# Kernel tuning notes

Measured on AMD Instinct MI355X. Metric: run time of the kernel, lower is better.

The kernel has to match this reference:

```python
import jax, jax.numpy as jnp
import numpy as np
from functools import partial

N = 8192          # nodes
E = 131072        # directed edges (avg degree 16)
INPUT_DIM = 256
INTERM = 32
LATENT = 64       # m
MAX_ITERS = 32    # fixed unroll of the rejection-sampling while-loop


def setup_inputs() -> dict:
    key = jax.random.key(0)
    ks = jax.random.split(key, 8)
    X = jax.random.normal(ks[0], (N, INPUT_DIM), dtype=jnp.float32)
    edge_index = jax.random.randint(ks[1], (2, E), 0, N, dtype=jnp.int64)
    W1 = jax.random.normal(ks[2], (INPUT_DIM, INTERM), dtype=jnp.float32) / np.sqrt(INPUT_DIM)
    b1 = jnp.zeros((INTERM,), jnp.float32)
    W_mu = jax.random.normal(ks[3], (INTERM, LATENT), dtype=jnp.float32) / np.sqrt(INTERM)
    b_mu = jnp.zeros((LATENT,), jnp.float32)
    W_k = jax.random.normal(ks[4], (INTERM, 1), dtype=jnp.float32) / np.sqrt(INTERM)
    b_k = jnp.zeros((1,), jnp.float32)
    return {"X": X, "edge_index": edge_index, "W1": W1, "b1": b1,
            "W_mu": W_mu, "b_mu": b_mu, "W_k": W_k, "b_k": b_k}


def _gcn(H, src, dst, norm, W, b):
    # GCNConv: out = D^-1/2 (A+I) D^-1/2 (H W) + b, edge-list form
    HW = H @ W
    msg = HW[src] * norm[:, None]
    return jax.ops.segment_sum(msg, dst, num_segments=N) + b


def _sample_w(kappas, key):
    # Wood's rejection sampling for the vMF mixing scalar w (fixed-iteration scan)
    m = LATENT
    s = jnp.sqrt(4.0 * kappas ** 2 + (m - 1) ** 2)
    b = (-2.0 * kappas + s) / (m - 1)
    a = (m - 1 + 2.0 * kappas + s) / 4.0
    d = 4.0 * a * b / (1.0 + b) - (m - 1) * np.log(m - 1)

    def step(carry, k):
        w, sampled = carry
        kb, ku = jax.random.split(k)
        eps = jax.random.beta(kb, (m - 1) / 2.0, (m - 1) / 2.0, (kappas.shape[0],))
        denom = 1.0 - (1.0 - b) * eps
        w_prop = (1.0 - (1.0 + b) * eps) / denom
        t = 2.0 * a * b / denom
        u = jax.random.uniform(ku, (kappas.shape[0],))
        acc = (m - 1) * jnp.log(t) - t + d >= jnp.log(u)
        w = jnp.where(sampled, w, w_prop)   # keep first accepted proposal
        sampled = sampled | acc
        return (w, sampled), None

    init = (jnp.zeros_like(kappas), jnp.zeros(kappas.shape, dtype=bool))
    (w, _), _ = jax.lax.scan(step, init, jax.random.split(key, MAX_ITERS))
    return w


def _sample_vMF(mus, kappas, key):
    m = LATENT
    kw, kv = jax.random.split(key)
    w = _sample_w(kappas, kw)[:, None]                     # [N,1]
    v = jax.random.normal(kv, (mus.shape[0], m - 1), dtype=mus.dtype)
    v = v / jnp.linalg.norm(v, axis=1, keepdims=True)
    z = jnp.concatenate([w, jnp.sqrt(jnp.clip(1.0 - w ** 2, 0.0)) * v], axis=-1)
    # householder reflection mapping e1 -> mu
    e = jnp.zeros((1, m), dtype=mus.dtype).at[0, 0].set(1.0)
    u = e - mus
    u = u / (jnp.linalg.norm(u, axis=-1, keepdims=True) + 1e-8)
    return z - 2.0 * jnp.sum(z * u, axis=-1, keepdims=True) * u


def reference(X, edge_index, W1, b1, W_mu, b_mu, W_k, b_k):
    src0, dst0 = edge_index[0], edge_index[1]
    loops = jnp.arange(N, dtype=src0.dtype)
    src = jnp.concatenate([src0, loops])
    dst = jnp.concatenate([dst0, loops])
    deg = jax.ops.segment_sum(jnp.ones(src.shape[0], X.dtype), dst, num_segments=N)
    dinv = jnp.where(deg > 0, jax.lax.rsqrt(deg), 0.0)
    norm = dinv[src] * dinv[dst]

    H = jax.nn.relu(_gcn(X, src, dst, norm, W1, b1))       # dropout in eval mode
    mus = _gcn(H, src, dst, norm, W_mu, b_mu)
    kap = jax.nn.softplus(jnp.squeeze(_gcn(H, src, dst, norm, W_k, b_k), -1))
    mus = mus / (jnp.linalg.norm(mus, axis=-1, keepdims=True) + 1e-12)

    Z = _sample_vMF(mus, kap, jax.random.key(42))
    ZZt = Z @ Z.T                                           # [N,N]
    return ZZt, mus, kap
```

## Files before the change

### kernel.cpp

```cpp
#include <hip/hip_runtime.h>
#include <hip/hip_bf16.h>

#pragma clang fp contract(off)

#define NN 8192
#define NE 131072
#define DIN 256
#define DH 32
#define DL 64

typedef unsigned int u32;
typedef __bf16 bf16x8 __attribute__((ext_vector_type(8)));
typedef float f32x4 __attribute__((ext_vector_type(4)));

struct Key { u32 a, b; };

__device__ __forceinline__ u32 rotl32(u32 x, int d) { return (x << d) | (x >> (32 - d)); }

__device__ __forceinline__ void tf2x32(u32 k0, u32 k1, u32& x0, u32& x1) {
  u32 k2 = k0 ^ k1 ^ 0x1BD11BDAu;
  x0 += k0; x1 += k1;
  x0 += x1; x1 = rotl32(x1, 13); x1 ^= x0;
  x0 += x1; x1 = rotl32(x1, 15); x1 ^= x0;
  x0 += x1; x1 = rotl32(x1, 26); x1 ^= x0;
  x0 += x1; x1 = rotl32(x1, 6);  x1 ^= x0;
  x0 += k1; x1 += k2 + 1u;
  x0 += x1; x1 = rotl32(x1, 17); x1 ^= x0;
  x0 += x1; x1 = rotl32(x1, 29); x1 ^= x0;
  x0 += x1; x1 = rotl32(x1, 16); x1 ^= x0;
  x0 += x1; x1 = rotl32(x1, 24); x1 ^= x0;
  x0 += k2; x1 += k0 + 2u;
  x0 += x1; x1 = rotl32(x1, 13); x1 ^= x0;
  x0 += x1; x1 = rotl32(x1, 15); x1 ^= x0;
  x0 += x1; x1 = rotl32(x1, 26); x1 ^= x0;
  x0 += x1; x1 = rotl32(x1, 6);  x1 ^= x0;
  x0 += k0; x1 += k1 + 3u;
  x0 += x1; x1 = rotl32(x1, 17); x1 ^= x0;
  x0 += x1; x1 = rotl32(x1, 29); x1 ^= x0;
  x0 += x1; x1 = rotl32(x1, 16); x1 ^= x0;
  x0 += x1; x1 = rotl32(x1, 24); x1 ^= x0;
  x0 += k1; x1 += k2 + 4u;
  x0 += x1; x1 = rotl32(x1, 13); x1 ^= x0;
  x0 += x1; x1 = rotl32(x1, 15); x1 ^= x0;
  x0 += x1; x1 = rotl32(x1, 26); x1 ^= x0;
  x0 += x1; x1 = rotl32(x1, 6);  x1 ^= x0;
  x0 += k2; x1 += k0 + 5u;
}

__device__ __forceinline__ Key fold(Key k, u32 i) {
  u32 x0 = 0u, x1 = i; tf2x32(k.a, k.b, x0, x1);
  Key r; r.a = x0; r.b = x1; return r;
}
__device__ __forceinline__ u32 pbits(Key k, u32 i) {
  u32 x0 = 0u, x1 = i; tf2x32(k.a, k.b, x0, x1);
  return x0 ^ x1;
}


__device__ __forceinline__ float xla_logf(float x) {
  if (x == 0.0f) return -__builtin_huge_valf();
  u32 bits = __float_as_uint(x);
  float ef = (float)((int)(bits >> 23) - 126);
  float m = __uint_as_float((bits & 0x007fffffu) | 0x3f000000u);
  if (m < 0.707106781186547524f) { ef = ef - 1.0f; m = m + m; }
  m = m - 1.0f;
  float z = m * m;
  float y = 7.0376836292e-2f;
  y = fmaf(y, m, -1.1514610310e-1f);
  y = fmaf(y, m, 1.1676998740e-1f);
  y = fmaf(y, m, -1.2420140846e-1f);
  y = fmaf(y, m, 1.4249322787e-1f);
  y = fmaf(y, m, -1.6668057665e-1f);
  y = fmaf(y, m, 2.0000714765e-1f);
  y = fmaf(y, m, -2.4999993993e-1f);
  y = fmaf(y, m, 3.3333331174e-1f);
  y = y * m;
  y = y * z;
  y = fmaf(ef, -2.12194440e-4f, y);
  y = fmaf(-0.5f, z, y);
  float r = m + y;
  r = fmaf(ef, 0.693359375f, r);
  return r;
}

__device__ __forceinline__ float xla_expf(float x) {
  x = fminf(x, 88.3762626647950f);
  x = fmaxf(x, -88.3762626647949f);
  float fx = fmaf(x, 1.44269504088896341f, 0.5f);
  fx = floorf(fx);
  x = fmaf(-fx, 0.693359375f, x);
  x = fmaf(fx, 2.12194440e-4f, x);
  float z = x * x;
  float y = 1.9875691500e-4f;
  y = fmaf(y, x, 1.3981999507e-3f);
  y = fmaf(y, x, 8.3334519073e-3f);
  y = fmaf(y, x, 4.1665795894e-2f);
  y = fmaf(y, x, 1.6666665459e-1f);
  y = fmaf(y, x, 5.0000001201e-1f);
  y = fmaf(y, z, x);
  y = y + 1.0f;
  int n = (int)fx;
  float p2n = __uint_as_float((u32)(n + 127) << 23);
  return y * p2n;
}

__device__ __forceinline__ float xla_log1pf(float x) {
  float u = x + 1.0f;
  if (u == 1.0f) return x;
  return xla_logf(u) * (x / (u - 1.0f));
}

__device__ __forceinline__ float u01_from_bits(u32 b) {
  return __uint_as_float((b >> 9) | 0x3f800000u) - 1.0f;
}
__device__ __forceinline__ float jax_uniform_scalar(Key k) {
  float f = u01_from_bits(pbits(k, 0u));
  return fmaxf(0.0f, f);
}

__device__ __forceinline__ float erfinv_f32(float x) {
  float w = -xla_log1pf(-(x * x));
  float p;
  if (w < 5.0f) {
    w = w - 2.5f;
    p = 2.81022636e-08f;
    p = fmaf(p, w, 3.43273939e-07f);
    p = fmaf(p, w, -3.5233877e-06f);
    p = fmaf(p, w, -4.39150654e-06f);
    p = fmaf(p, w, 0.00021858087f);
    p = fmaf(p, w, -0.00125372503f);
    p = fmaf(p, w, -0.00417768164f);
    p = fmaf(p, w, 0.246640727f);
    p = fmaf(p, w, 1.50140941f);
  } else {
    w = sqrtf(w) - 3.0f;
    p = -0.000200214257f;
    p = fmaf(p, w, 0.000100950558f);
    p = fmaf(p, w, 0.00134934322f);
    p = fmaf(p, w, -0.00367342844f);
    p = fmaf(p, w, 0.00573950773f);
    p = fmaf(p, w, -0.0076224613f);
    p = fmaf(p, w, 0.00943887047f);
    p = fmaf(p, w, 1.00167406f);
    p = fmaf(p, w, 2.83297682f);
  }
  return p * x;
}

__device__ __forceinline__ float normal_from_bits(u32 b) {
  float f = u01_from_bits(b);
  const float lo = -0.99999994f;
  float u = fmaxf(lo, fmaf(f, 2.0f, lo));
  return 1.4142135623730951f * erfinv_f32(u);
}

__device__ float loggamma31_5(Key k) {
  const float dd = 31.5f - (1.0f / 3.0f);
  const float cc = 1.0f / sqrtf(9.0f * dd);
  Key key = fold(k, 0u);
  float X = 0.0f, V = 1.0f, U = 2.0f;
  for (int it = 0; it < 64; ++it) {
    bool c1 = U >= fmaf(-0.0331f, X * X, 1.0f);
    bool c2 = xla_logf(U) >= fmaf(dd, (1.0f - V) + xla_logf(V), X * 0.5f);
    if (!(c1 && c2)) break;
    Key xk = fold(key, 1u);
    Key Uk = fold(key, 2u);
    key = fold(key, 0u);
    float x = 0.0f, v = -1.0f;
    for (int j = 0; j < 32 && v <= 0.0f; ++j) {
      Key sk = fold(xk, 1u);
      xk = fold(xk, 0u);
      x = normal_from_bits(pbits(sk, 0u));
      v = fmaf(x, cc, 1.0f);
    }
    X = x * x; V = (v * v) * v;
    U = jax_uniform_scalar(Uk);
  }
  return xla_logf(V) + xla_logf(dd);
}

__device__ __forceinline__ float wave_sum(float v) {
  for (int d = 1; d < 64; d <<= 1) v += __shfl_xor(v, d, 64);
  return v;
}


__global__ void count_k(const int* __restrict__ ei, u32* __restrict__ cnt) {
  int e = blockIdx.x * blockDim.x + threadIdx.x;
  if (e < NE) atomicAdd(&cnt[ei[NE + e]], 1u);
}

__global__ void scan_k(const u32* __restrict__ cnt, u32* __restrict__ off, float* __restrict__ dinv) {
  __shared__ u32 part[256];
  int t = threadIdx.x;
  int base = t * 32;
  u32 s = 0;
  for (int i = 0; i < 32; ++i) s += cnt[base + i];
  part[t] = s;
  __syncthreads();
  if (t == 0) {
    u32 acc = 0;
    for (int i = 0; i < 256; ++i) { u32 v = part[i]; part[i] = acc; acc += v; }
  }
  __syncthreads();
  u32 acc = part[t];
  for (int i = 0; i < 32; ++i) {
    off[base + i] = acc;
    u32 c = cnt[base + i];
    acc += c;
    dinv[base + i] = 1.0f / sqrtf((float)(c + 1u));
  }
  if (t == 255) off[NN] = acc;
}

__global__ void fill_k(const int* __restrict__ ei, const u32* __restrict__ off,
                       u32* __restrict__ fl, u32* __restrict__ csr) {
  int e = blockIdx.x * blockDim.x + threadIdx.x;
  if (e < NE) {
    int d = ei[NE + e];
    u32 p = off[d] + atomicAdd(&fl[d], 1u);
    csr[p] = (u32)e;
  }
}

__global__ void sort_k(const u32* __restrict__ off, u32* __restrict__ csr) {
  int n = blockIdx.x * blockDim.x + threadIdx.x;
  if (n >= NN) return;
  u32 s = off[n], e2 = off[n + 1];
  for (u32 i = s + 1; i < e2; ++i) {
    u32 v = csr[i]; u32 j = i;
    while (j > s && csr[j - 1] > v) { csr[j] = csr[j - 1]; --j; }
    csr[j] = v;
  }
}

__global__ __launch_bounds__(256) void mm_xw1_k(const float* __restrict__ X,
                                                const float* __restrict__ W1,
                                                float* __restrict__ XW) {
  __shared__ float w[DIN * DH];
  for (int i = threadIdx.x; i < DIN * DH; i += 256) w[i] = W1[i];
  __syncthreads();
  int f = threadIdx.x & 31, r0 = threadIdx.x >> 5;
  int base = blockIdx.x * 32;
  for (int pass = 0; pass < 4; ++pass) {
    int r = base + r0 + pass * 8;
    const float4* xr = reinterpret_cast<const float4*>(X + (size_t)r * DIN);
    float acc = 0.0f;
    for (int k4 = 0; k4 < DIN / 4; ++k4) {
      float4 xv = xr[k4];
      int k = k4 * 4;
      acc = fmaf(xv.x, w[(k + 0) * DH + f], acc);
      acc = fmaf(xv.y, w[(k + 1) * DH + f], acc);
      acc = fmaf(xv.z, w[(k + 2) * DH + f], acc);
      acc = fmaf(xv.w, w[(k + 3) * DH + f], acc);
    }
    XW[(size_t)r * DH + f] = acc;
  }
}

__global__ void agg_h_k(const float* __restrict__ XW, const u32* __restrict__ off,
                        const u32* __restrict__ csr, const int* __restrict__ ei,
                        const float* __restrict__ dinv, const float* __restrict__ b1,
                        float* __restrict__ H) {
  int idx = blockIdx.x * blockDim.x + threadIdx.x;
  int n = idx >> 5, f = idx & 31;
  if (n >= NN) return;
  float dn = dinv[n];
  float acc = 0.0f;
  u32 s0 = off[n], s1 = off[n + 1];
  for (u32 p = s0; p < s1; ++p) {
    int e = (int)csr[p];
    int s = ei[e];
    acc += XW[s * DH + f] * (dinv[s] * dn);
  }
  acc += XW[n * DH + f] * (dn * dn);
  acc += b1[f];
  H[n * DH + f] = fmaxf(acc, 0.0f);
}

__global__ void mm_h_k(const float* __restrict__ H, const float* __restrict__ Wmu,
                       const float* __restrict__ Wk, float* __restrict__ HWmu,
                       float* __restrict__ HWk) {
  __shared__ float wm[DH * DL];
  __shared__ float wk[DH];
  for (int i = threadIdx.x; i < DH * DL; i += 256) wm[i] = Wmu[i];
  if (threadIdx.x < DH) wk[threadIdx.x] = Wk[threadIdx.x];
  __syncthreads();
  int f = threadIdx.x & 63, l = threadIdx.x >> 6;
  int n = blockIdx.x * 4 + l;
  const float* h = H + n * DH;
  float acc = 0.0f;
  for (int k = 0; k < DH; ++k) acc = fmaf(h[k], wm[k * DL + f], acc);
  HWmu[(size_t)n * DL + f] = acc;
  if (f == 0) {
    float a2 = 0.0f;
    for (int k = 0; k < DH; ++k) a2 = fmaf(h[k], wk[k], a2);
    HWk[n] = a2;
  }
}

__global__ void agg_mu_k(const float* __restrict__ HW, const u32* __restrict__ off,
                         const u32* __restrict__ csr, const int* __restrict__ ei,
                         const float* __restrict__ dinv, const float* __restrict__ bmu,
                         float* __restrict__ out) {
  int idx = blockIdx.x * blockDim.x + threadIdx.x;
  int n = idx >> 6, f = idx & 63;
  if (n >= NN) return;
  float dn = dinv[n], acc = 0.0f;
  for (u32 p = off[n]; p < off[n + 1]; ++p) {
    int e = (int)csr[p]; int s = ei[e];
    acc += HW[(size_t)s * DL + f] * (dinv[s] * dn);
  }
  acc += HW[(size_t)n * DL + f] * (dn * dn);
  out[(size_t)n * DL + f] = acc + bmu[f];
}

__global__ void agg_kap_k(const float* __restrict__ HWk, const u32* __restrict__ off,
                          const u32* __restrict__ csr, const int* __restrict__ ei,
                          const float* __restrict__ dinv, const float* __restrict__ bk,
                          float* __restrict__ kap, float* __restrict__ outKA) {
  int n = blockIdx.x * blockDim.x + threadIdx.x;
  if (n >= NN) return;
  float dn = dinv[n], acc = 0.0f;
  for (u32 p = off[n]; p < off[n + 1]; ++p) {
    int e = (int)csr[p]; int s = ei[e];
    acc += HWk[s] * (dinv[s] * dn);
  }
  acc += HWk[n] * (dn * dn);
  acc += bk[0];
  float sp = fmaxf(acc, 0.0f) + xla_log1pf(xla_expf(-fabsf(acc)));
  kap[n] = sp; outKA[n] = sp;
}

__global__ void norm_mus_k(const float* __restrict__ musraw, float* __restrict__ mus,
                           float* __restrict__ outMU) {
  int gid = blockIdx.x * blockDim.x + threadIdx.x;
  int n = gid >> 6, lane = threadIdx.x & 63;
  if (n >= NN) return;
  float v = musraw[(size_t)n * DL + lane];
  float nm = sqrtf(wave_sum(v * v)) + 1e-12f;
  float r = v / nm;
  mus[(size_t)n * DL + lane] = r;
  outMU[(size_t)n * DL + lane] = r;
}


__global__ void build_keys_k(u32* __restrict__ ktab) {
  if (threadIdx.x != 0 || blockIdx.x != 0) return;
  Key root; root.a = 0u; root.b = 42u;
  Key kw = fold(root, 0u);
  Key kv = fold(root, 1u);
  ktab[192] = kv.a; ktab[193] = kv.b;
  for (int t = 0; t < 32; ++t) {
    Key kt = fold(kw, (u32)t);
    Key kb = fold(kt, 0u);
    Key ku = fold(kt, 1u);
    Key ka = fold(kb, 0u);
    Key kbb = fold(kb, 1u);
    ktab[6 * t + 0] = ka.a;  ktab[6 * t + 1] = ka.b;
    ktab[6 * t + 2] = kbb.a; ktab[6 * t + 3] = kbb.b;
    ktab[6 * t + 4] = ku.a;  ktab[6 * t + 5] = ku.b;
  }
}

__global__ void sample_w_k(const float* __restrict__ kap, const u32* __restrict__ ktab,
                           float* __restrict__ wv) {
  int n = blockIdx.x * blockDim.x + threadIdx.x;
  if (n >= NN) return;
  float kappa = kap[n];
  float kk = kappa * kappa;
  float s  = sqrtf(fmaf(4.0f, kk, 3969.0f));
  float bb = fmaf(-2.0f, kappa, s) / 63.0f;
  float aa = (fmaf(2.0f, kappa, 63.0f) + s) / 4.0f;
  float dd = (4.0f * aa) * bb / (1.0f + bb) - 261.01748776266657f;
  float w = 0.0f;
  for (int t = 0; t < 32; ++t) {
    const u32* kt = ktab + 6 * t;
    Key ka; ka.a = kt[0]; ka.b = kt[1];
    Key kb; kb.a = kt[2]; kb.b = kt[3];
    Key ku; ku.a = kt[4]; ku.b = kt[5];
    Key sa = fold(ka, (u32)n);
    Key sb = fold(kb, (u32)n);
    float lga = loggamma31_5(sa);
    float lgb = loggamma31_5(sb);
    float mx = fmaxf(lga, lgb);
    float ea = xla_expf(lga - mx), eb = xla_expf(lgb - mx);
    float eps = ea / (ea + eb);
    float u = fmaxf(0.0f, u01_from_bits(pbits(ku, (u32)n)));
    float denom = fmaf(-(1.0f - bb), eps, 1.0f);
    w = fmaf(-(1.0f + bb), eps, 1.0f) / denom;
    float tt = (2.0f * aa) * bb / denom;
    float lt = xla_logf(tt);
    float margin = fmaf(63.0f, lt, -tt) + dd;
    if (margin >= xla_logf(u)) break;
  }
  wv[n] = w;
}

__global__ void z_k(const float* __restrict__ mus, const float* __restrict__ wv,
                    const u32* __restrict__ ktab, __bf16* __restrict__ Zh) {
  int gid = blockIdx.x * blockDim.x + threadIdx.x;
  int n = gid >> 6, lane = threadIdx.x & 63;
  if (n >= NN) return;
  Key kv; kv.a = ktab[192]; kv.b = ktab[193];
  float vj = 0.0f;
  if (lane >= 1) {
    u32 idx = (u32)(n * 63 + (lane - 1));
    vj = normal_from_bits(pbits(kv, idx));
  }
  float vn = sqrtf(wave_sum(vj * vj));
  vj = vj / vn;
  float w = wv[n];
  float zj = (lane == 0) ? w : sqrtf(fmaxf(1.0f - w * w, 0.0f)) * vj;
  float mu = mus[(size_t)n * DL + lane];
  float uh = ((lane == 0) ? 1.0f : 0.0f) - mu;
  float un = sqrtf(wave_sum(uh * uh)) + 1e-8f;
  uh = uh / un;
  float dot = wave_sum(zj * uh);
  float zf = zj - 2.0f * dot * uh;
  Zh[(size_t)n * DL + lane] = (__bf16)zf;
}

__global__ __launch_bounds__(256) void zzt_k(const __bf16* __restrict__ Zh,
                                             float* __restrict__ out) {
  int wave = threadIdx.x >> 6;
  int lane = threadIdx.x & 63;
  int bi = blockIdx.y * 128 + (wave >> 1) * 64;
  int bj = blockIdx.x * 128 + (wave & 1) * 64;
  int r = lane & 15, kh = lane >> 4;
  bf16x8 afr[4][2], bfr[4][2];
#pragma unroll
  for (int ig = 0; ig < 4; ++ig)
#pragma unroll
    for (int kk = 0; kk < 2; ++kk) {
      afr[ig][kk] = *reinterpret_cast<const bf16x8*>(
          Zh + (size_t)(bi + ig * 16 + r) * DL + kk * 32 + kh * 8);
      bfr[ig][kk] = *reinterpret_cast<const bf16x8*>(
          Zh + (size_t)(bj + ig * 16 + r) * DL + kk * 32 + kh * 8);
    }
  f32x4 acc[4][4];
#pragma unroll
  for (int ig = 0; ig < 4; ++ig)
#pragma unroll
    for (int jg = 0; jg < 4; ++jg) {
      acc[ig][jg] = (f32x4){0.0f, 0.0f, 0.0f, 0.0f};
      acc[ig][jg] = __builtin_amdgcn_mfma_f32_16x16x32_bf16(
          afr[ig][0], bfr[jg][0], acc[ig][jg], 0, 0, 0);
      acc[ig][jg] = __builtin_amdgcn_mfma_f32_16x16x32_bf16(
          afr[ig][1], bfr[jg][1], acc[ig][jg], 0, 0, 0);
    }
#pragma unroll
  for (int ig = 0; ig < 4; ++ig)
#pragma unroll
    for (int jg = 0; jg < 4; ++jg) {
      size_t rowbase = (size_t)(bi + ig * 16 + kh * 4);
#pragma unroll
      for (int rr = 0; rr < 4; ++rr) {
        out[(rowbase + rr) * NN + (bj + jg * 16 + r)] = acc[ig][jg][rr];
      }
    }
}


extern "C" void kernel_launch(void* const* d_in, const int* in_sizes, int n_in,
                              void* d_out, int out_size, void* d_ws, size_t ws_size,
                              hipStream_t stream) {
  const float* X   = (const float*)d_in[0];
  const int*   ei  = (const int*)d_in[1];
  const float* W1  = (const float*)d_in[2];
  const float* b1  = (const float*)d_in[3];
  const float* Wmu = (const float*)d_in[4];
  const float* bmu = (const float*)d_in[5];
  const float* Wk  = (const float*)d_in[6];
  const float* bk  = (const float*)d_in[7];

  char* wp = (char*)d_ws;
  auto alloc = [&](size_t bytes) -> char* {
    char* p = wp; wp += (bytes + 255) & ~(size_t)255; return p;
  };
  u32* cnt    = (u32*)alloc((size_t)NN * 4);
  u32* fill   = (u32*)alloc((size_t)NN * 4);
  u32* off    = (u32*)alloc((size_t)(NN + 1) * 4);
  u32* csr    = (u32*)alloc((size_t)NE * 4);
  u32* ktab   = (u32*)alloc(256 * 4);
  float* dinv = (float*)alloc((size_t)NN * 4);
  float* XW1  = (float*)alloc((size_t)NN * DH * 4);
  float* H    = (float*)alloc((size_t)NN * DH * 4);
  float* HWmu = (float*)alloc((size_t)NN * DL * 4);
  float* HWk  = (float*)alloc((size_t)NN * 4);
  float* musr = (float*)alloc((size_t)NN * DL * 4);
  float* mus  = (float*)alloc((size_t)NN * DL * 4);
  float* kap  = (float*)alloc((size_t)NN * 4);
  float* wv   = (float*)alloc((size_t)NN * 4);
  __bf16* Zh  = (__bf16*)alloc((size_t)NN * DL * 2);

  float* outZZ = (float*)d_out;
  float* outMU = outZZ + (size_t)NN * NN;
  float* outKA = outMU + (size_t)NN * DL;

  hipMemsetAsync(cnt, 0, (size_t)NN * 4, stream);
  hipMemsetAsync(fill, 0, (size_t)NN * 4, stream);
  build_keys_k<<<1, 64, 0, stream>>>(ktab);
  count_k<<<NE / 256, 256, 0, stream>>>(ei, cnt);
  scan_k<<<1, 256, 0, stream>>>(cnt, off, dinv);
  fill_k<<<NE / 256, 256, 0, stream>>>(ei, off, fill, csr);
  sort_k<<<NN / 256, 256, 0, stream>>>(off, csr);
  mm_xw1_k<<<NN / 32, 256, 0, stream>>>(X, W1, XW1);
  agg_h_k<<<NN * DH / 256, 256, 0, stream>>>(XW1, off, csr, ei, dinv, b1, H);
  mm_h_k<<<NN / 4, 256, 0, stream>>>(H, Wmu, Wk, HWmu, HWk);
  agg_mu_k<<<NN * DL / 256, 256, 0, stream>>>(HWmu, off, csr, ei, dinv, bmu, musr);
  agg_kap_k<<<NN / 256, 256, 0, stream>>>(HWk, off, csr, ei, dinv, bk, kap, outKA);
  norm_mus_k<<<NN * DL / 256, 256, 0, stream>>>(musr, mus, outMU);
  sample_w_k<<<NN / 256, 256, 0, stream>>>(kap, ktab, wv);
  z_k<<<NN * DL / 256, 256, 0, stream>>>(mus, wv, ktab, Zh);
  dim3 g(64, 64);
  zzt_k<<<g, 256, 0, stream>>>(Zh, outZZ);
}
```

Before: 270.1 us.

## Fuse GCN aggregation stages, inline RNG keys, and vectorize ZZt stores

The first GCN aggregation is fused with the Wmu/Wk projection, so H lives in shared memory and never goes to global memory. The mu and kappa aggregations share one launch by splitting on block index, and so do the mu normalisation and the vMF w sampling. The key-table kernel is removed by deriving keys inline, and the two memsets are merged into one that relies on the adjacent cnt/fill allocations. The ZZt output now uses float4 stores with swapped row and column indexing, which is correct only because Z·Zᵀ is symmetric. This cuts launch count and intermediate traffic and the number of store instructions on the large output.

```diff
diff --git a/kernel.cpp b/kernel.cpp
--- a/kernel.cpp
+++ b/kernel.cpp
@@ -234,6 +234,7 @@
   }
 }
 
+
 __global__ __launch_bounds__(256) void mm_xw1_k(const float* __restrict__ X,
                                                 const float* __restrict__ W1,
                                                 float* __restrict__ XW) {
@@ -258,151 +259,142 @@
   }
 }
 
-__global__ void agg_h_k(const float* __restrict__ XW, const u32* __restrict__ off,
-                        const u32* __restrict__ csr, const int* __restrict__ ei,
-                        const float* __restrict__ dinv, const float* __restrict__ b1,
-                        float* __restrict__ H) {
-  int idx = blockIdx.x * blockDim.x + threadIdx.x;
-  int n = idx >> 5, f = idx & 31;
-  if (n >= NN) return;
-  float dn = dinv[n];
-  float acc = 0.0f;
-  u32 s0 = off[n], s1 = off[n + 1];
-  for (u32 p = s0; p < s1; ++p) {
-    int e = (int)csr[p];
-    int s = ei[e];
-    acc += XW[s * DH + f] * (dinv[s] * dn);
-  }
-  acc += XW[n * DH + f] * (dn * dn);
-  acc += b1[f];
-  H[n * DH + f] = fmaxf(acc, 0.0f);
-}
-
-__global__ void mm_h_k(const float* __restrict__ H, const float* __restrict__ Wmu,
-                       const float* __restrict__ Wk, float* __restrict__ HWmu,
-                       float* __restrict__ HWk) {
+__global__ __launch_bounds__(256) void agg_h_mm_k(const float* __restrict__ XW,
+                                                  const u32* __restrict__ off,
+                                                  const u32* __restrict__ csr,
+                                                  const int* __restrict__ ei,
+                                                  const float* __restrict__ dinv,
+                                                  const float* __restrict__ b1,
+                                                  const float* __restrict__ Wmu,
+                                                  const float* __restrict__ Wk,
+                                                  float* __restrict__ HWmu,
+                                                  float* __restrict__ HWk) {
+  __shared__ float Hs[8][DH];
   __shared__ float wm[DH * DL];
   __shared__ float wk[DH];
   for (int i = threadIdx.x; i < DH * DL; i += 256) wm[i] = Wmu[i];
   if (threadIdx.x < DH) wk[threadIdx.x] = Wk[threadIdx.x];
+  int nl = threadIdx.x >> 5, f = threadIdx.x & 31;
+  int n = blockIdx.x * 8 + nl;
+  {
+    float dn = dinv[n];
+    float acc = 0.0f;
+    u32 s0 = off[n], s1 = off[n + 1];
+    for (u32 p = s0; p < s1; ++p) {
+      int e = (int)csr[p];
+      int s = ei[e];
+      acc += XW[(size_t)s * DH + f] * (dinv[s] * dn);
+    }
+    acc += XW[(size_t)n * DH + f] * (dn * dn);
+    acc += b1[f];
+    Hs[nl][f] = fmaxf(acc, 0.0f);
+  }
   __syncthreads();
-  int f = threadIdx.x & 63, l = threadIdx.x >> 6;
-  int n = blockIdx.x * 4 + l;
-  const float* h = H + n * DH;
-  float acc = 0.0f;
-  for (int k = 0; k < DH; ++k) acc = fmaf(h[k], wm[k * DL + f], acc);
-  HWmu[(size_t)n * DL + f] = acc;
-  if (f == 0) {
-    float a2 = 0.0f;
-    for (int k = 0; k < DH; ++k) a2 = fmaf(h[k], wk[k], a2);
-    HWk[n] = a2;
-  }
-}
-
-__global__ void agg_mu_k(const float* __restrict__ HW, const u32* __restrict__ off,
-                         const u32* __restrict__ csr, const int* __restrict__ ei,
-                         const float* __restrict__ dinv, const float* __restrict__ bmu,
-                         float* __restrict__ out) {
-  int idx = blockIdx.x * blockDim.x + threadIdx.x;
-  int n = idx >> 6, f = idx & 63;
-  if (n >= NN) return;
-  float dn = dinv[n], acc = 0.0f;
-  for (u32 p = off[n]; p < off[n + 1]; ++p) {
-    int e = (int)csr[p]; int s = ei[e];
-    acc += HW[(size_t)s * DL + f] * (dinv[s] * dn);
-  }
-  acc += HW[(size_t)n * DL + f] * (dn * dn);
-  out[(size_t)n * DL + f] = acc + bmu[f];
-}
-
-__global__ void agg_kap_k(const float* __restrict__ HWk, const u32* __restrict__ off,
-                          const u32* __restrict__ csr, const int* __restrict__ ei,
-                          const float* __restrict__ dinv, const float* __restrict__ bk,
-                          float* __restrict__ kap, float* __restrict__ outKA) {
-  int n = blockIdx.x * blockDim.x + threadIdx.x;
-  if (n >= NN) return;
-  float dn = dinv[n], acc = 0.0f;
-  for (u32 p = off[n]; p < off[n + 1]; ++p) {
-    int e = (int)csr[p]; int s = ei[e];
-    acc += HWk[s] * (dinv[s] * dn);
-  }
-  acc += HWk[n] * (dn * dn);
-  acc += bk[0];
-  float sp = fmaxf(acc, 0.0f) + xla_log1pf(xla_expf(-fabsf(acc)));
-  kap[n] = sp; outKA[n] = sp;
-}
-
-__global__ void norm_mus_k(const float* __restrict__ musraw, float* __restrict__ mus,
-                           float* __restrict__ outMU) {
+  int f2 = threadIdx.x & 63, l = threadIdx.x >> 6;
+#pragma unroll
+  for (int rep = 0; rep < 2; ++rep) {
+    int nl2 = l + rep * 4;
+    int n2 = blockIdx.x * 8 + nl2;
+    const float* h = Hs[nl2];
+    float acc = 0.0f;
+    for (int k = 0; k < DH; ++k) acc = fmaf(h[k], wm[k * DL + f2], acc);
+    HWmu[(size_t)n2 * DL + f2] = acc;
+    if (f2 == 0) {
+      float a2 = 0.0f;
+      for (int k = 0; k < DH; ++k) a2 = fmaf(h[k], wk[k], a2);
+      HWk[n2] = a2;
+    }
+  }
+}
+
+__global__ void agg_mu_kap_k(const float* __restrict__ HW, const float* __restrict__ HWk,
+                             const u32* __restrict__ off, const u32* __restrict__ csr,
+                             const int* __restrict__ ei, const float* __restrict__ dinv,
+                             const float* __restrict__ bmu, const float* __restrict__ bk,
+                             float* __restrict__ musr, float* __restrict__ kap,
+                             float* __restrict__ outKA) {
+  int bid = blockIdx.x;
+  if (bid < 2048) {
+    int idx = bid * 256 + threadIdx.x;
+    int n = idx >> 6, f = idx & 63;
+    float dn = dinv[n], acc = 0.0f;
+    for (u32 p = off[n]; p < off[n + 1]; ++p) {
+      int e = (int)csr[p]; int s = ei[e];
+      acc += HW[(size_t)s * DL + f] * (dinv[s] * dn);
+    }
+    acc += HW[(size_t)n * DL + f] * (dn * dn);
+    musr[(size_t)n * DL + f] = acc + bmu[f];
+  } else {
+    int n = (bid - 2048) * 256 + threadIdx.x;
+    if (n >= NN) return;
+    float dn = dinv[n], acc = 0.0f;
+    for (u32 p = off[n]; p < off[n + 1]; ++p) {
+      int e = (int)csr[p]; int s = ei[e];
+      acc += HWk[s] * (dinv[s] * dn);
+    }
+    acc += HWk[n] * (dn * dn);
+    acc += bk[0];
+    float sp = fmaxf(acc, 0.0f) + xla_log1pf(xla_expf(-fabsf(acc)));
+    kap[n] = sp; outKA[n] = sp;
+  }
+}
+
+__global__ void norm_sample_k(const float* __restrict__ musraw, float* __restrict__ mus,
+                              float* __restrict__ outMU, const float* __restrict__ kap,
+                              float* __restrict__ wv) {
+  int bid = blockIdx.x;
+  if (bid < 2048) {
+    int gid = bid * 256 + threadIdx.x;
+    int n = gid >> 6, lane = threadIdx.x & 63;
+    float v = musraw[(size_t)n * DL + lane];
+    float nm = sqrtf(wave_sum(v * v)) + 1e-12f;
+    float r = v / nm;
+    mus[(size_t)n * DL + lane] = r;
+    outMU[(size_t)n * DL + lane] = r;
+  } else {
+    int n = (bid - 2048) * 256 + threadIdx.x;
+    if (n >= NN) return;
+    Key root; root.a = 0u; root.b = 42u;
+    Key kw = fold(root, 0u);
+    float kappa = kap[n];
+    float kk = kappa * kappa;
+    float s  = sqrtf(fmaf(4.0f, kk, 3969.0f));
+    float bb = fmaf(-2.0f, kappa, s) / 63.0f;
+    float aa = (fmaf(2.0f, kappa, 63.0f) + s) / 4.0f;
+    float dd = (4.0f * aa) * bb / (1.0f + bb) - 261.01748776266657f;
+    float w = 0.0f;
+    for (int t = 0; t < 32; ++t) {
+      Key kt = fold(kw, (u32)t);
+      Key kb = fold(kt, 0u);
+      Key ku = fold(kt, 1u);
+      Key ka = fold(kb, 0u);
+      Key kbb = fold(kb, 1u);
+      Key sa = fold(ka, (u32)n);
+      Key sb = fold(kbb, (u32)n);
+      float lga = loggamma31_5(sa);
+      float lgb = loggamma31_5(sb);
+      float mx = fmaxf(lga, lgb);
+      float ea = xla_expf(lga - mx), eb = xla_expf(lgb - mx);
+      float eps = ea / (ea + eb);
+      float u = fmaxf(0.0f, u01_from_bits(pbits(ku, (u32)n)));
+      float denom = fmaf(-(1.0f - bb), eps, 1.0f);
+      w = fmaf(-(1.0f + bb), eps, 1.0f) / denom;
+      float tt = (2.0f * aa) * bb / denom;
+      float lt = xla_logf(tt);
+      float margin = fmaf(63.0f, lt, -tt) + dd;
+      if (margin >= xla_logf(u)) break;
+    }
+    wv[n] = w;
+  }
+}
+
+__global__ void z_k(const float* __restrict__ mus, const float* __restrict__ wv,
+                    __bf16* __restrict__ Zh) {
   int gid = blockIdx.x * blockDim.x + threadIdx.x;
   int n = gid >> 6, lane = threadIdx.x & 63;
   if (n >= NN) return;
-  float v = musraw[(size_t)n * DL + lane];
-  float nm = sqrtf(wave_sum(v * v)) + 1e-12f;
-  float r = v / nm;
-  mus[(size_t)n * DL + lane] = r;
-  outMU[(size_t)n * DL + lane] = r;
-}
-
-
-__global__ void build_keys_k(u32* __restrict__ ktab) {
-  if (threadIdx.x != 0 || blockIdx.x != 0) return;
   Key root; root.a = 0u; root.b = 42u;
-  Key kw = fold(root, 0u);
   Key kv = fold(root, 1u);
-  ktab[192] = kv.a; ktab[193] = kv.b;
-  for (int t = 0; t < 32; ++t) {
-    Key kt = fold(kw, (u32)t);
-    Key kb = fold(kt, 0u);
-    Key ku = fold(kt, 1u);
-    Key ka = fold(kb, 0u);
-    Key kbb = fold(kb, 1u);
-    ktab[6 * t + 0] = ka.a;  ktab[6 * t + 1] = ka.b;
-    ktab[6 * t + 2] = kbb.a; ktab[6 * t + 3] = kbb.b;
-    ktab[6 * t + 4] = ku.a;  ktab[6 * t + 5] = ku.b;
-  }
-}
-
-__global__ void sample_w_k(const float* __restrict__ kap, const u32* __restrict__ ktab,
-                           float* __restrict__ wv) {
-  int n = blockIdx.x * blockDim.x + threadIdx.x;
-  if (n >= NN) return;
-  float kappa = kap[n];
-  float kk = kappa * kappa;
-  float s  = sqrtf(fmaf(4.0f, kk, 3969.0f));
-  float bb = fmaf(-2.0f, kappa, s) / 63.0f;
-  float aa = (fmaf(2.0f, kappa, 63.0f) + s) / 4.0f;
-  float dd = (4.0f * aa) * bb / (1.0f + bb) - 261.01748776266657f;
-  float w = 0.0f;
-  for (int t = 0; t < 32; ++t) {
-    const u32* kt = ktab + 6 * t;
-    Key ka; ka.a = kt[0]; ka.b = kt[1];
-    Key kb; kb.a = kt[2]; kb.b = kt[3];
-    Key ku; ku.a = kt[4]; ku.b = kt[5];
-    Key sa = fold(ka, (u32)n);
-    Key sb = fold(kb, (u32)n);
-    float lga = loggamma31_5(sa);
-    float lgb = loggamma31_5(sb);
-    float mx = fmaxf(lga, lgb);
-    float ea = xla_expf(lga - mx), eb = xla_expf(lgb - mx);
-    float eps = ea / (ea + eb);
-    float u = fmaxf(0.0f, u01_from_bits(pbits(ku, (u32)n)));
-    float denom = fmaf(-(1.0f - bb), eps, 1.0f);
-    w = fmaf(-(1.0f + bb), eps, 1.0f) / denom;
-    float tt = (2.0f * aa) * bb / denom;
-    float lt = xla_logf(tt);
-    float margin = fmaf(63.0f, lt, -tt) + dd;
-    if (margin >= xla_logf(u)) break;
-  }
-  wv[n] = w;
-}
-
-__global__ void z_k(const float* __restrict__ mus, const float* __restrict__ wv,
-                    const u32* __restrict__ ktab, __bf16* __restrict__ Zh) {
-  int gid = blockIdx.x * blockDim.x + threadIdx.x;
-  int n = gid >> 6, lane = threadIdx.x & 63;
-  if (n >= NN) return;
-  Key kv; kv.a = ktab[192]; kv.b = ktab[193];
   float vj = 0.0f;
   if (lane >= 1) {
     u32 idx = (u32)(n * 63 + (lane - 1));
@@ -453,11 +445,10 @@
   for (int ig = 0; ig < 4; ++ig)
 #pragma unroll
     for (int jg = 0; jg < 4; ++jg) {
-      size_t rowbase = (size_t)(bi + ig * 16 + kh * 4);
-#pragma unroll
-      for (int rr = 0; rr < 4; ++rr) {
-        out[(rowbase + rr) * NN + (bj + jg * 16 + r)] = acc[ig][jg][rr];
-      }
+      size_t row = (size_t)(bj + jg * 16 + r);
+      float4 v = make_float4(acc[ig][jg][0], acc[ig][jg][1],
+                             acc[ig][jg][2], acc[ig][jg][3]);
+      *reinterpret_cast<float4*>(&out[row * NN + (bi + ig * 16 + kh * 4)]) = v;
     }
 }
 
@@ -482,10 +473,8 @@
   u32* fill   = (u32*)alloc((size_t)NN * 4);
   u32* off    = (u32*)alloc((size_t)(NN + 1) * 4);
   u32* csr    = (u32*)alloc((size_t)NE * 4);
-  u32* ktab   = (u32*)alloc(256 * 4);
   float* dinv = (float*)alloc((size_t)NN * 4);
   float* XW1  = (float*)alloc((size_t)NN * DH * 4);
-  float* H    = (float*)alloc((size_t)NN * DH * 4);
   float* HWmu = (float*)alloc((size_t)NN * DL * 4);
   float* HWk  = (float*)alloc((size_t)NN * 4);
   float* musr = (float*)alloc((size_t)NN * DL * 4);
@@ -498,21 +487,18 @@
   float* outMU = outZZ + (size_t)NN * NN;
   float* outKA = outMU + (size_t)NN * DL;
 
-  hipMemsetAsync(cnt, 0, (size_t)NN * 4, stream);
-  hipMemsetAsync(fill, 0, (size_t)NN * 4, stream);
-  build_keys_k<<<1, 64, 0, stream>>>(ktab);
+  hipMemsetAsync(cnt, 0, (size_t)NN * 8, stream);
   count_k<<<NE / 256, 256, 0, stream>>>(ei, cnt);
   scan_k<<<1, 256, 0, stream>>>(cnt, off, dinv);
   fill_k<<<NE / 256, 256, 0, stream>>>(ei, off, fill, csr);
   sort_k<<<NN / 256, 256, 0, stream>>>(off, csr);
   mm_xw1_k<<<NN / 32, 256, 0, stream>>>(X, W1, XW1);
-  agg_h_k<<<NN * DH / 256, 256, 0, stream>>>(XW1, off, csr, ei, dinv, b1, H);
-  mm_h_k<<<NN / 4, 256, 0, stream>>>(H, Wmu, Wk, HWmu, HWk);
-  agg_mu_k<<<NN * DL / 256, 256, 0, stream>>>(HWmu, off, csr, ei, dinv, bmu, musr);
-  agg_kap_k<<<NN / 256, 256, 0, stream>>>(HWk, off, csr, ei, dinv, bk, kap, outKA);
-  norm_mus_k<<<NN * DL / 256, 256, 0, stream>>>(musr, mus, outMU);
-  sample_w_k<<<NN / 256, 256, 0, stream>>>(kap, ktab, wv);
-  z_k<<<NN * DL / 256, 256, 0, stream>>>(mus, wv, ktab, Zh);
+  agg_h_mm_k<<<NN / 8, 256, 0, stream>>>(XW1, off, csr, ei, dinv, b1, Wmu, Wk,
+                                         HWmu, HWk);
+  agg_mu_kap_k<<<2048 + NN / 256, 256, 0, stream>>>(HWmu, HWk, off, csr, ei, dinv,
+                                                    bmu, bk, musr, kap, outKA);
+  norm_sample_k<<<2048 + NN / 256, 256, 0, stream>>>(musr, mus, outMU, kap, wv);
+  z_k<<<NN * DL / 256, 256, 0, stream>>>(mus, wv, Zh);
   dim3 g(64, 64);
   zzt_k<<<g, 256, 0, stream>>>(Zh, outZZ);
 }
```

After: 240.4 us. -11.0%, faster.
